# Kernel optimization log

Hardware: AMD Instinct MI355X
Metric: run time of the kernel (lower is better)

The kernel has to match this reference:

```python
import jax, jax.numpy as jnp
import numpy as np

VOCAB = 90000
MAX_ID = 95000
EFFECT_DIM = 758
ADD_DIM = 10
EMBED_DIM = 768  # EFFECT_DIM + ADD_DIM
CTX = 1024
MAX_SYN = 8


def setup_inputs() -> dict:
    key = jax.random.key(0)
    k_ids, k_emb, k_rev, k_tab, k_msk = jax.random.split(key, 5)
    ids = jax.random.randint(k_ids, (CTX,), 0, VOCAB, dtype=jnp.int64)
    W_emb = jax.random.normal(k_emb, (MAX_ID, EFFECT_DIM), dtype=jnp.float32)
    W_rev = jax.random.normal(k_rev, (EMBED_DIM, MAX_ID), dtype=jnp.float32)
    padding = 0.1 * jnp.ones((CTX, ADD_DIM), dtype=jnp.float32)
    # synonym ids live in [VOCAB, MAX_ID); only some slots are active (variable-length lists)
    syn_table = jax.random.randint(k_tab, (MAX_ID, MAX_SYN), VOCAB, MAX_ID, dtype=jnp.int32)
    syn_mask = jax.random.randint(k_msk, (MAX_ID, MAX_SYN), 0, 2, dtype=jnp.int32)
    # tokens >= VOCAB (synonym ids themselves) have no synonyms
    syn_mask = syn_mask.at[VOCAB:].set(0)
    return {"ids": ids, "W_emb": W_emb, "W_rev": W_rev, "padding": padding,
            "syn_table": syn_table, "syn_mask": syn_mask}


def reference(ids, W_emb, W_rev, padding, syn_table, syn_mask):
    # VirtualEmbedding: base gather + masked synonym gather/scale/accumulate.
    # i_sum is computed BEFORE the synonym loop in the original, so each
    # synonym contribution is independent -> vectorized masked reduction.
    # (Dropout in eval mode is the identity.)
    base = W_emb[ids]                              # [L, D]
    syn_ids = syn_table[ids]                       # [L, K]
    syn = W_emb[syn_ids]                           # [L, K, D]
    mask = syn_mask[ids].astype(base.dtype)        # [L, K]
    i_sum = jnp.sum(base, axis=-1, keepdims=True)  # [L, 1]
    s_sum = jnp.sum(syn, axis=-1)                  # [L, K]
    d = i_sum / s_sum                              # [L, K]
    emb = base + jnp.einsum('lk,lkd->ld', mask * d, syn)
    # concat fixed context padding, then ReverseEmbedding projection to vocab
    full = jnp.concatenate([emb, padding], axis=1)  # [L, EMBED_DIM]
    return full @ W_rev                             # [L, MAX_ID]
```

## Files before the change

### kernel.cpp

```cpp
#include <hip/hip_runtime.h>
#include <stdint.h>

#define EFFECT_DIM 758
#define ADD_DIM 10
#define EMBED_DIM 768
#define NCOLS 95000
#define NSYN 8
#define NROWS 1024
#define NT256 372
#define TILE_B 32768

typedef __attribute__((ext_vector_type(8))) __bf16 bf16x8;
typedef __attribute__((ext_vector_type(16))) float f32x16;
typedef __attribute__((ext_vector_type(4))) uint32_t u32x4;


static __device__ __forceinline__ uint32_t pack2(float a, float b) {
  uint32_t r;
  asm("v_cvt_pk_bf16_f32 %0, %1, %2" : "=v"(r) : "v"(a), "v"(b));
  return r;
}

#define GLOAD16(src, dst)                                                   \
  __builtin_amdgcn_global_load_lds(                                         \
      (const __attribute__((address_space(1))) uint32_t*)(src),             \
      (__attribute__((address_space(3))) uint32_t*)(dst), 16, 0, 0)

__global__ __launch_bounds__(256) void emb_kernel(
    const int* __restrict__ ids, const float* __restrict__ W_emb,
    const float* __restrict__ padding, const int* __restrict__ syn_table,
    const int* __restrict__ syn_mask, char* __restrict__ ws)
{
  const int l = blockIdx.x;
  const int t = threadIdx.x;
  const int id = ids[l];
  int sid[NSYN];
  int msk[NSYN];
#pragma unroll
  for (int k = 0; k < NSYN; ++k) {
    sid[k] = syn_table[id * NSYN + k];
    msk[k] = syn_mask[id * NSYN + k];
  }

  double p[9] = {0, 0, 0, 0, 0, 0, 0, 0, 0};
  for (int d = t; d < EFFECT_DIM; d += 256) {
    p[0] += (double)W_emb[(size_t)id * EFFECT_DIM + d];
#pragma unroll
    for (int k = 0; k < NSYN; ++k)
      p[k + 1] += (double)W_emb[(size_t)sid[k] * EFFECT_DIM + d];
  }

  __shared__ double s_red[9][4];
  const int w = t >> 6;
#pragma unroll
  for (int k = 0; k < 9; ++k) {
    double v = p[k];
#pragma unroll
    for (int off = 32; off > 0; off >>= 1) v += __shfl_down(v, off, 64);
    if ((t & 63) == 0) s_red[k][w] = v;
  }
  __syncthreads();

  const double isum = s_red[0][0] + s_red[0][1] + s_red[0][2] + s_red[0][3];
  float coef[NSYN];
#pragma unroll
  for (int k = 0; k < NSYN; ++k) {
    double ss = s_red[k + 1][0] + s_red[k + 1][1] + s_red[k + 1][2] + s_red[k + 1][3];
    coef[k] = msk[k] ? (float)(isum / ss) : 0.0f;
  }

  const int r = l & 255;
  char* wbase = ws + (size_t)(l >> 8) * (12 * TILE_B);

  for (int j = t; j < 384; j += 256) {
    const int d0 = 2 * j;
    float v0, v1;
    if (d0 < EFFECT_DIM) {
      const float* bp = W_emb + (size_t)id * EFFECT_DIM + d0;
      v0 = bp[0];
      v1 = bp[1];
#pragma unroll
      for (int k = 0; k < NSYN; ++k) {
        const float* sp = W_emb + (size_t)sid[k] * EFFECT_DIM + d0;
        v0 = fmaf(coef[k], sp[0], v0);
        v1 = fmaf(coef[k], sp[1], v1);
      }
    } else {
      v0 = padding[l * ADD_DIM + (d0 - EFFECT_DIM)];
      v1 = padding[l * ADD_DIM + (d0 + 1 - EFFECT_DIM)];
    }
    const int ks   = j >> 5;
    const int jl   = j & 31;
    const int kk   = jl >> 3;
    const int byte = (jl & 7) * 4;
    const int lane = (r & 31) + ((byte >> 4) << 5);
    *(uint32_t*)(wbase + ks * TILE_B + kk * 8192 + (r >> 5) * 1024 +
                 lane * 16 + (byte & 15)) = pack2(v0, v1);
  }
}

__global__ __launch_bounds__(512, 2) void gemm_fused(
    const float* __restrict__ Wrev, const char* __restrict__ Abuf,
    float* __restrict__ out)
{
  extern __shared__ char lds[];
  const int t = threadIdx.x;
  const int l = t & 63;
  const int w = t >> 6;
  const int wm = w >> 2;
  const int wn = w & 3;

  const int wgid = blockIdx.x;
  const int xcd  = wgid & 7;
  const int work = xcd * 186 + (wgid >> 3);
  const int mt = work & 3;
  const int nt = work >> 2;
  const int n0 = nt * 256;

  const char* asrc = Abuf + (size_t)mt * (12 * TILE_B);

  const int sn = t & 255;
  const int kg = t >> 8;
  const int gn = n0 + sn;
  const bool valid = gn < NCOLS;

  float br[32];

#define AGLD(s, ksi)                                                         \
  {                                                                          \
    _Pragma("unroll") for (int kk = 0; kk < 4; ++kk)                         \
      GLOAD16(asrc + (ksi)*TILE_B + kk*8192 + t*16,                          \
              lds + (s)*65536 + kk*8192 + w*1024);                           \
  }

#define BLOAD(ksi)                                                           \
  {                                                                          \
    const float* p = Wrev + (size_t)((ksi)*64 + kg*32) * NCOLS + gn;         \
    _Pragma("unroll") for (int j = 0; j < 32; ++j)                           \
      br[j] = valid ? p[(size_t)j * NCOLS] : 0.0f;                           \
  }

#define BSTORE(s)                                                            \
  {                                                                          \
    _Pragma("unroll") for (int c = 0; c < 2; ++c) {                          \
      u32x4 u0, u1;                                                          \
      _Pragma("unroll") for (int j = 0; j < 4; ++j) {                        \
        u0[j] = pack2(br[c*16 + 2*j],     br[c*16 + 2*j + 1]);               \
        u1[j] = pack2(br[c*16 + 8 + 2*j], br[c*16 + 9 + 2*j]);               \
      }                                                                      \
      char* bb = lds + (s)*65536 + 32768 + (kg*2 + c)*8192 + (sn>>5)*1024;   \
      *(u32x4*)(bb + (sn & 31)*16) = u0;                                     \
      *(u32x4*)(bb + ((sn & 31) + 32)*16) = u1;                              \
    }                                                                        \
  }

  AGLD(0, 0);
  BLOAD(0);
  BSTORE(0);
  asm volatile("s_waitcnt vmcnt(0) lgkmcnt(0)" ::: "memory");
  __builtin_amdgcn_s_barrier();

  f32x16 acc[4][2] = {};

  for (int T = 0; T < 12; ++T) {
    const int cs = T & 1;
    const int Tn = (T < 11) ? T + 1 : 11;

    __builtin_amdgcn_sched_barrier(0);
    AGLD(cs ^ 1, Tn);
    BLOAD(Tn);
    __builtin_amdgcn_sched_barrier(0);

    const char* aw = lds + cs * 65536 + (wm * 4) * 1024 + l * 16;
    const char* bw = lds + cs * 65536 + 32768 + (wn * 2) * 1024 + l * 16;

#pragma unroll
    for (int p = 0; p < 4; ++p) {
      bf16x8 a[4], b[2];
#pragma unroll
      for (int mr = 0; mr < 4; ++mr)
        a[mr] = *(const bf16x8*)(aw + p * 8192 + mr * 1024);
#pragma unroll
      for (int nr = 0; nr < 2; ++nr)
        b[nr] = *(const bf16x8*)(bw + p * 8192 + nr * 1024);
      __builtin_amdgcn_s_setprio(1);
#pragma unroll
      for (int mr = 0; mr < 4; ++mr)
#pragma unroll
        for (int nr = 0; nr < 2; ++nr)
          acc[mr][nr] = __builtin_amdgcn_mfma_f32_32x32x16_bf16(
              a[mr], b[nr], acc[mr][nr], 0, 0, 0);
      __builtin_amdgcn_s_setprio(0);
    }

    __builtin_amdgcn_sched_barrier(0);
    BSTORE(cs ^ 1);
    asm volatile("s_waitcnt lgkmcnt(0)" ::: "memory");
    __builtin_amdgcn_sched_barrier(0);
    __builtin_amdgcn_s_barrier();
  }
#undef AGLD
#undef BLOAD
#undef BSTORE

  const int lh = l >> 5;
#pragma unroll
  for (int nr = 0; nr < 2; ++nr) {
    const int gc = n0 + wn * 64 + nr * 32 + (l & 31);
    if (gc < NCOLS) {
#pragma unroll
      for (int mr = 0; mr < 4; ++mr)
#pragma unroll
        for (int reg = 0; reg < 16; ++reg) {
          const int row = mt * 256 + wm * 128 + mr * 32 +
                          (reg & 3) + 8 * (reg >> 2) + 4 * lh;
          out[(size_t)row * NCOLS + gc] = acc[mr][nr][reg];
        }
    }
  }
}

extern "C" void kernel_launch(void* const* d_in, const int* in_sizes, int n_in,
                              void* d_out, int out_size, void* d_ws, size_t ws_size,
                              hipStream_t stream) {
  const int*   ids       = (const int*)d_in[0];
  const float* W_emb     = (const float*)d_in[1];
  const float* W_rev     = (const float*)d_in[2];
  const float* padding   = (const float*)d_in[3];
  const int*   syn_table = (const int*)d_in[4];
  const int*   syn_mask  = (const int*)d_in[5];
  float* out = (float*)d_out;
  char*  ws  = (char*)d_ws;

  hipLaunchKernelGGL(emb_kernel, dim3(NROWS), dim3(256), 0, stream,
                     ids, W_emb, padding, syn_table, syn_mask, ws);

  hipLaunchKernelGGL(gemm_fused, dim3(4 * NT256), dim3(512), 131072, stream,
                     W_rev, ws, out);
}
```

Measured before the change: 343.4 us.

## Double-buffer W_rev register prefetch two K-steps ahead in fused GEMM

The GEMM main loop is unrolled into pairs of steps that alternate between two register buffers for the W_rev tile. Global loads for step T+2 are now issued while step T computes, and explicit vmcnt waits let the newest batch stay in flight across the barrier. The goal is to hide more of the global load latency of the strided fp32 W_rev reads behind MFMA work. The cost is 32 extra VGPRs per thread on top of 128 accumulator registers, which may cause spills or lower occupancy. The hand-counted vmcnt values also make the loop sensitive to how many loads the compiler emits.

```diff
diff --git a/kernel.cpp b/kernel.cpp
--- a/kernel.cpp
+++ b/kernel.cpp
@@ -124,7 +124,7 @@
   const int gn = n0 + sn;
   const bool valid = gn < NCOLS;
 
-  float br[32];
+  float br0[32], br1[32];
 
 #define AGLD(s, ksi)                                                         \
   {                                                                          \
@@ -133,14 +133,14 @@
               lds + (s)*65536 + kk*8192 + w*1024);                           \
   }
 
-#define BLOAD(ksi)                                                           \
+#define BLOAD(br, ksi)                                                       \
   {                                                                          \
     const float* p = Wrev + (size_t)((ksi)*64 + kg*32) * NCOLS + gn;         \
     _Pragma("unroll") for (int j = 0; j < 32; ++j)                           \
       br[j] = valid ? p[(size_t)j * NCOLS] : 0.0f;                           \
   }
 
-#define BSTORE(s)                                                            \
+#define BSTORE(br, s)                                                        \
   {                                                                          \
     _Pragma("unroll") for (int c = 0; c < 2; ++c) {                          \
       u32x4 u0, u1;                                                          \
@@ -154,51 +154,59 @@
     }                                                                        \
   }
 
+#define COMPUTE(cs)                                                          \
+  {                                                                          \
+    const char* aw = lds + (cs)*65536 + (wm*4)*1024 + l*16;                  \
+    const char* bw = lds + (cs)*65536 + 32768 + (wn*2)*1024 + l*16;          \
+    _Pragma("unroll") for (int p = 0; p < 4; ++p) {                          \
+      bf16x8 a[4], b[2];                                                     \
+      _Pragma("unroll") for (int mr = 0; mr < 4; ++mr)                       \
+        a[mr] = *(const bf16x8*)(aw + p*8192 + mr*1024);                     \
+      _Pragma("unroll") for (int nr = 0; nr < 2; ++nr)                       \
+        b[nr] = *(const bf16x8*)(bw + p*8192 + nr*1024);                     \
+      __builtin_amdgcn_s_setprio(1);                                         \
+      _Pragma("unroll") for (int mr = 0; mr < 4; ++mr)                       \
+        _Pragma("unroll") for (int nr = 0; nr < 2; ++nr)                     \
+          acc[mr][nr] = __builtin_amdgcn_mfma_f32_32x32x16_bf16(             \
+              a[mr], b[nr], acc[mr][nr], 0, 0, 0);                           \
+      __builtin_amdgcn_s_setprio(0);                                         \
+    }                                                                        \
+  }
+
+#define STEP(cs, TT, brCur, brNext)                                          \
+  {                                                                          \
+    if ((TT) + 1 < 12) AGLD((cs) ^ 1, (TT) + 1);        \
+    if ((TT) + 2 < 12) BLOAD(brNext, (TT) + 2);                              \
+    __builtin_amdgcn_sched_barrier(0);                                       \
+    COMPUTE(cs);                                                             \
+    __builtin_amdgcn_sched_barrier(0);                                       \
+    if ((TT) + 1 < 12) {                                                     \
+      BSTORE(brCur, (cs) ^ 1);             \
+      asm volatile("s_waitcnt lgkmcnt(0)" ::: "memory");                     \
+      if ((TT) + 2 < 12) asm volatile("s_waitcnt vmcnt(32)" ::: "memory");   \
+      else               asm volatile("s_waitcnt vmcnt(0)" ::: "memory");    \
+      __builtin_amdgcn_sched_barrier(0);                                     \
+      __builtin_amdgcn_s_barrier();                                          \
+    }                                                                        \
+  }
+
   AGLD(0, 0);
-  BLOAD(0);
-  BSTORE(0);
-  asm volatile("s_waitcnt vmcnt(0) lgkmcnt(0)" ::: "memory");
+  BLOAD(br0, 0);
+  BSTORE(br0, 0);
+  BLOAD(br0, 1);
+  asm volatile("s_waitcnt lgkmcnt(0)" ::: "memory");
+  __builtin_amdgcn_sched_barrier(0);
   __builtin_amdgcn_s_barrier();
 
   f32x16 acc[4][2] = {};
 
-  for (int T = 0; T < 12; ++T) {
-    const int cs = T & 1;
-    const int Tn = (T < 11) ? T + 1 : 11;
-
-    __builtin_amdgcn_sched_barrier(0);
-    AGLD(cs ^ 1, Tn);
-    BLOAD(Tn);
-    __builtin_amdgcn_sched_barrier(0);
-
-    const char* aw = lds + cs * 65536 + (wm * 4) * 1024 + l * 16;
-    const char* bw = lds + cs * 65536 + 32768 + (wn * 2) * 1024 + l * 16;
-
-#pragma unroll
-    for (int p = 0; p < 4; ++p) {
-      bf16x8 a[4], b[2];
-#pragma unroll
-      for (int mr = 0; mr < 4; ++mr)
-        a[mr] = *(const bf16x8*)(aw + p * 8192 + mr * 1024);
-#pragma unroll
-      for (int nr = 0; nr < 2; ++nr)
-        b[nr] = *(const bf16x8*)(bw + p * 8192 + nr * 1024);
-      __builtin_amdgcn_s_setprio(1);
-#pragma unroll
-      for (int mr = 0; mr < 4; ++mr)
-#pragma unroll
-        for (int nr = 0; nr < 2; ++nr)
-          acc[mr][nr] = __builtin_amdgcn_mfma_f32_32x32x16_bf16(
-              a[mr], b[nr], acc[mr][nr], 0, 0, 0);
-      __builtin_amdgcn_s_setprio(0);
-    }
-
-    __builtin_amdgcn_sched_barrier(0);
-    BSTORE(cs ^ 1);
-    asm volatile("s_waitcnt lgkmcnt(0)" ::: "memory");
-    __builtin_amdgcn_sched_barrier(0);
-    __builtin_amdgcn_s_barrier();
-  }
+#pragma unroll
+  for (int Ti = 0; Ti < 6; ++Ti) {
+    STEP(0, 2 * Ti,     br0, br1);
+    STEP(1, 2 * Ti + 1, br1, br0);
+  }
+#undef STEP
+#undef COMPUTE
 #undef AGLD
 #undef BLOAD
 #undef BSTORE
```

New measurement: 329.6 us, median of 2. -4.0%, faster.
